# Kernel optimization log

Measured on AMD Instinct MI355X. Metric: run time of the kernel, lower is better.

The kernel has to match this reference:

```python
import jax, jax.numpy as jnp
import numpy as np

B, S, HID, NH, HD, RD, RATIO = 2, 4096, 2048, 16, 128, 64, 4
THETA = 10000.0


def _rope_tables(positions, rd, theta):
    # Unique per-pair frequencies: first half of the Llama cat([freqs, freqs], -1).
    half = rd // 2
    inv_freq = 1.0 / (theta ** (jnp.arange(half, dtype=jnp.float32) / half))
    ang = positions.astype(jnp.float32)[:, None] * inv_freq[None, :]  # [L, half]
    return jnp.cos(ang), jnp.sin(ang)


def _apply_partial_rope_interleaved(x, cos, sin, rd):
    # x: [B, H, L, D]; rotate last rd dims, pairs (2k, 2k+1). cos/sin: [L, rd//2]
    nope, rope = x[..., :-rd], x[..., -rd:]
    pr = rope.reshape(rope.shape[:-1] + (rd // 2, 2))
    a, b = pr[..., 0], pr[..., 1]
    c = cos[None, None]  # [1,1,L,half]
    s = sin[None, None]
    new = jnp.stack([a * c - b * s, a * s + b * c], axis=-1).reshape(rope.shape)
    return jnp.concatenate([nope, new], axis=-1)


def _pool_overlap(kv, gate, ape, ratio, hd):
    # kv/gate: [B, L, 2*hd]; ape: [ratio, 2*hd]. Softmax-gated sum-pool with
    # cross-window overlap: each window pools 2*ratio raw slots (prev window's
    # first-half features + current window's second-half features).
    b, length, feat = kv.shape
    n_w = length // ratio
    kv_w = kv.reshape(b, n_w, ratio, feat)
    gate_w = gate.reshape(b, n_w, ratio, feat) + ape

    def remap(t, fill):
        cur = t[..., hd:]                          # [b, n_w, ratio, hd]
        prev = t[:, :-1, :, :hd]                   # window N-1 first half
        pad = jnp.full((b, 1, ratio, hd), fill, t.dtype)
        prev = jnp.concatenate([pad, prev], axis=1)
        return jnp.concatenate([prev, cur], axis=2)  # [b, n_w, 2*ratio, hd]

    kv_o = remap(kv_w, 0.0)
    gate_o = remap(gate_w, -jnp.inf)
    w = jax.nn.softmax(gate_o, axis=2)
    return (kv_o * w).sum(axis=2)  # [b, n_w, hd]


def setup_inputs() -> dict:
    key = jax.random.key(0)
    ks = jax.random.split(key, 7)
    sc = lambda d: 1.0 / np.sqrt(d)
    return {
        "hidden": jax.random.normal(ks[0], (B, S, HID), jnp.float32),
        "wq": jax.random.normal(ks[1], (HID, NH * HD), jnp.float32) * sc(HID),
        "wkv": jax.random.normal(ks[2], (HID, 2 * HD), jnp.float32) * sc(HID),
        "wgate": jax.random.normal(ks[3], (HID, 2 * HD), jnp.float32) * sc(HID),
        "ape": jax.random.normal(ks[4], (RATIO, 2 * HD), jnp.float32) * 0.02,
        "sinks": jax.random.normal(ks[5], (NH,), jnp.float32) * 0.02,
        "wo": jax.random.normal(ks[6], (NH * HD, HID), jnp.float32) * sc(NH * HD),
        "ratio": RATIO,
        "head_dim": HD,
        "rope_head_dim": RD,
        "num_heads": NH,
    }


def reference(hidden, wq, wkv, wgate, ape, sinks, wo, ratio, head_dim, rope_head_dim, num_heads):
    b, s, _ = hidden.shape
    scale = head_dim ** -0.5

    # Projections
    q = (hidden @ wq).reshape(b, s, num_heads, head_dim).transpose(0, 2, 1, 3)  # [b,h,s,d]
    kv = hidden @ wkv      # [b, s, 2*d]
    gate = hidden @ wgate  # [b, s, 2*d]

    # Overlap gated pooling -> compressed shared KV  [b, n_w, d]
    pooled = _pool_overlap(kv, gate, ape, ratio, head_dim)
    n_w = pooled.shape[1]

    # Partial interleaved RoPE; pooled positions = w * ratio (pool_base = 0)
    q_pos = jnp.arange(s)
    k_pos = jnp.arange(n_w) * ratio
    cq, sq = _rope_tables(q_pos, rope_head_dim, THETA)
    ck, sk = _rope_tables(k_pos, rope_head_dim, THETA)
    q_rot = _apply_partial_rope_interleaved(q, cq, sq, rope_head_dim)
    k_rot = _apply_partial_rope_interleaved(pooled[:, None], ck, sk, rope_head_dim)[:, 0]  # [b,n_w,d]
    v = pooled  # [b, n_w, d]

    # Causal mask over compressed windows: query t sees window w iff its last
    # raw token (w+1)*ratio - 1 <= t.
    mask = jnp.where(q_pos[:, None] >= k_pos[None, :] + ratio - 1, 0.0, -jnp.inf)  # [s, n_w]

    scores = jnp.einsum("bhqd,bkd->bhqk", q_rot, k_rot) * scale + mask[None, None]
    sink_col = jnp.broadcast_to(sinks.reshape(1, num_heads, 1, 1), (b, num_heads, s, 1))
    combined = jnp.concatenate([scores, sink_col], axis=-1)
    probs = jax.nn.softmax(combined - jax.lax.stop_gradient(combined.max(axis=-1, keepdims=True)), axis=-1)[..., :-1]

    attn = jnp.einsum("bhqk,bkd->bhqd", probs, v)               # [b,h,s,d]
    out = attn.transpose(0, 2, 1, 3).reshape(b, s, num_heads * head_dim) @ wo
    return out
```

## Files before the change

kernel.cpp:

```cpp
#include <hip/hip_runtime.h>
#include <math.h>

typedef unsigned short u16;
typedef unsigned int   u32;
typedef __bf16 bf16x8 __attribute__((ext_vector_type(8)));
typedef float  f32x4  __attribute__((ext_vector_type(4)));

#define S_LEN 4096
#define HID   2048
#define NHEAD 16
#define HD    128
#define NW    1024
#define TOK   8192
#define LN10000 9.2103403719761836f
#define NEG_BIG (-1e30f)

__device__ __forceinline__ float b2f(u16 u){
  union { u32 i; float f; } v; v.i = ((u32)u) << 16; return v.f;
}
__device__ __forceinline__ u16 f2b(float f){
  union { float f; u32 i; } v; v.f = f;
  return (u16)((v.i + 0x7FFFu + ((v.i >> 16) & 1u)) >> 16);
}

__global__ __launch_bounds__(256) void cvt_bf16(const float* __restrict__ in,
                                                u16* __restrict__ out){
  size_t i = (size_t)blockIdx.x*256 + threadIdx.x;
  float4 a = ((const float4*)in)[2*i];
  float4 b = ((const float4*)in)[2*i+1];
  u16 t[8];
  t[0]=f2b(a.x); t[1]=f2b(a.y); t[2]=f2b(a.z); t[3]=f2b(a.w);
  t[4]=f2b(b.x); t[5]=f2b(b.y); t[6]=f2b(b.z); t[7]=f2b(b.w);
  *(uint4*)&out[i*8] = *(uint4*)t;
}

__global__ __launch_bounds__(256) void transpose_w(const float* __restrict__ in,
    u16* __restrict__ out, int K, int N){
  __shared__ float t[32][33];
  const int n0 = blockIdx.x*32, k0 = blockIdx.y*32;
  const int c = threadIdx.x & 31, r8 = threadIdx.x >> 5;
  #pragma unroll
  for (int i = 0; i < 4; i++)
    t[r8 + i*8][c] = in[(size_t)(k0 + r8 + i*8)*N + n0 + c];
  __syncthreads();
  #pragma unroll
  for (int i = 0; i < 4; i++)
    out[(size_t)(n0 + r8 + i*8)*K + k0 + c] = f2b(t[c][r8 + i*8]);
}

typedef __attribute__((address_space(3))) u16 as3_u16;
typedef __attribute__((address_space(1))) const u16 as1_u16;
__device__ __forceinline__ void gload16(const u16* g, u16* l){
  __builtin_amdgcn_global_load_lds((as1_u16*)g, (as3_u16*)l, 16, 0, 0);
}

template<typename TC>
__global__ __launch_bounds__(512, 1) void gemm256(const u16* __restrict__ A,
    const u16* __restrict__ Bt, TC* __restrict__ C, int M, int N, int K)
{
  __shared__ __align__(16) u16 LA[2][256*64];
  __shared__ __align__(16) u16 LB[2][256*64];
  const int tid  = threadIdx.x;
  const int lane = tid & 63;
  const int w    = tid >> 6;
  const int wm   = w & 1;
  const int wn   = w >> 1;
  const int lrw  = lane & 15;
  const int quad = lane >> 4;
  const int NB   = N >> 8;
  const int nwg  = gridDim.x;
  const int bid  = blockIdx.x;
  const int swz  = (bid & 7) * (nwg >> 3) + (bid >> 3);
  const int bN   = (swz % NB) << 8;
  const int bM   = (swz / NB) << 8;

  const int rlo = lane >> 3;
  const int csw = ((lane & 7) ^ rlo) << 3;
  const int sr0 = w * 16;
  const int swr = (lrw & 7) << 3;
  const u16* Ag = A  + (size_t)bM * K + (size_t)rlo * K + csw;
  const u16* Bg = Bt + (size_t)bN * K + (size_t)rlo * K + csw;
  const size_t rK = (size_t)K;

  f32x4 acc[8][4];
  #pragma unroll
  for (int i = 0; i < 8; i++)
    #pragma unroll
    for (int j = 0; j < 4; j++)
      #pragma unroll
      for (int r = 0; r < 4; r++) acc[i][j][r] = 0.f;

  const int NT = K >> 6;

  gload16(Ag + (size_t)(  0 + sr0    )*rK, &LA[0][(  0 + sr0    )*64]);
  gload16(Ag + (size_t)(  0 + sr0 + 8)*rK, &LA[0][(  0 + sr0 + 8)*64]);
  gload16(Bg + (size_t)(  0 + sr0    )*rK, &LB[0][(  0 + sr0    )*64]);
  gload16(Bg + (size_t)(  0 + sr0 + 8)*rK, &LB[0][(  0 + sr0 + 8)*64]);
  gload16(Bg + (size_t)(128 + sr0    )*rK, &LB[0][(128 + sr0    )*64]);
  gload16(Bg + (size_t)(128 + sr0 + 8)*rK, &LB[0][(128 + sr0 + 8)*64]);
  gload16(Ag + (size_t)(128 + sr0    )*rK, &LA[0][(128 + sr0    )*64]);
  gload16(Ag + (size_t)(128 + sr0 + 8)*rK, &LA[0][(128 + sr0 + 8)*64]);
  asm volatile("s_waitcnt vmcnt(2)" ::: "memory");
  __builtin_amdgcn_s_barrier();
  __builtin_amdgcn_sched_barrier(0);

  for (int t = 0; t < NT; ++t){
    const int cur = t & 1, nxt = cur ^ 1;
    const int kn  = ((t + 1) & (NT - 1)) << 6;
    const u16* la = &LA[cur][0];
    const u16* lb = &LB[cur][0];
    u16* sa = &LA[nxt][0];
    u16* sb = &LB[nxt][0];

    bf16x8 bfr[4][2], afr[2][2];

    gload16(Ag + (size_t)(  0 + sr0    )*rK + kn, &sa[(  0 + sr0    )*64]);
    gload16(Ag + (size_t)(  0 + sr0 + 8)*rK + kn, &sa[(  0 + sr0 + 8)*64]);
    gload16(Bg + (size_t)(  0 + sr0    )*rK + kn, &sb[(  0 + sr0    )*64]);
    gload16(Bg + (size_t)(  0 + sr0 + 8)*rK + kn, &sb[(  0 + sr0 + 8)*64]);
    #pragma unroll
    for (int nf = 0; nf < 4; nf++)
      #pragma unroll
      for (int kh = 0; kh < 2; kh++)
        bfr[nf][kh] = *(const bf16x8*)&lb[(wn*16 + nf*64 + lrw)*64 + ((kh*32 + quad*8) ^ swr)];
    #pragma unroll
    for (int i = 0; i < 2; i++)
      #pragma unroll
      for (int kh = 0; kh < 2; kh++)
        afr[i][kh] = *(const bf16x8*)&la[(wm*16 + (0+i)*32 + lrw)*64 + ((kh*32 + quad*8) ^ swr)];
    __builtin_amdgcn_s_barrier();
    __builtin_amdgcn_sched_barrier(0);
    __builtin_amdgcn_s_setprio(1);
    #pragma unroll
    for (int i = 0; i < 2; i++)
      #pragma unroll
      for (int nf = 0; nf < 4; nf++)
        #pragma unroll
        for (int kh = 0; kh < 2; kh++)
          acc[0+i][nf] = __builtin_amdgcn_mfma_f32_16x16x32_bf16(afr[i][kh], bfr[nf][kh], acc[0+i][nf], 0, 0, 0);
    __builtin_amdgcn_s_setprio(0);
    __builtin_amdgcn_s_barrier();
    __builtin_amdgcn_sched_barrier(0);

    gload16(Bg + (size_t)(128 + sr0    )*rK + kn, &sb[(128 + sr0    )*64]);
    gload16(Bg + (size_t)(128 + sr0 + 8)*rK + kn, &sb[(128 + sr0 + 8)*64]);
    #pragma unroll
    for (int i = 0; i < 2; i++)
      #pragma unroll
      for (int kh = 0; kh < 2; kh++)
        afr[i][kh] = *(const bf16x8*)&la[(wm*16 + (2+i)*32 + lrw)*64 + ((kh*32 + quad*8) ^ swr)];
    asm volatile("s_waitcnt vmcnt(6)" ::: "memory");
    __builtin_amdgcn_s_barrier();
    __builtin_amdgcn_sched_barrier(0);
    __builtin_amdgcn_s_setprio(1);
    #pragma unroll
    for (int i = 0; i < 2; i++)
      #pragma unroll
      for (int nf = 0; nf < 4; nf++)
        #pragma unroll
        for (int kh = 0; kh < 2; kh++)
          acc[2+i][nf] = __builtin_amdgcn_mfma_f32_16x16x32_bf16(afr[i][kh], bfr[nf][kh], acc[2+i][nf], 0, 0, 0);
    __builtin_amdgcn_s_setprio(0);
    __builtin_amdgcn_s_barrier();
    __builtin_amdgcn_sched_barrier(0);

    gload16(Ag + (size_t)(128 + sr0    )*rK + kn, &sa[(128 + sr0    )*64]);
    gload16(Ag + (size_t)(128 + sr0 + 8)*rK + kn, &sa[(128 + sr0 + 8)*64]);
    #pragma unroll
    for (int i = 0; i < 2; i++)
      #pragma unroll
      for (int kh = 0; kh < 2; kh++)
        afr[i][kh] = *(const bf16x8*)&la[(wm*16 + (4+i)*32 + lrw)*64 + ((kh*32 + quad*8) ^ swr)];
    __builtin_amdgcn_s_barrier();
    __builtin_amdgcn_sched_barrier(0);
    __builtin_amdgcn_s_setprio(1);
    #pragma unroll
    for (int i = 0; i < 2; i++)
      #pragma unroll
      for (int nf = 0; nf < 4; nf++)
        #pragma unroll
        for (int kh = 0; kh < 2; kh++)
          acc[4+i][nf] = __builtin_amdgcn_mfma_f32_16x16x32_bf16(afr[i][kh], bfr[nf][kh], acc[4+i][nf], 0, 0, 0);
    __builtin_amdgcn_s_setprio(0);
    __builtin_amdgcn_s_barrier();
    __builtin_amdgcn_sched_barrier(0);

    #pragma unroll
    for (int i = 0; i < 2; i++)
      #pragma unroll
      for (int kh = 0; kh < 2; kh++)
        afr[i][kh] = *(const bf16x8*)&la[(wm*16 + (6+i)*32 + lrw)*64 + ((kh*32 + quad*8) ^ swr)];
    asm volatile("s_waitcnt vmcnt(2)" ::: "memory");
    __builtin_amdgcn_s_barrier();
    __builtin_amdgcn_sched_barrier(0);
    __builtin_amdgcn_s_setprio(1);
    #pragma unroll
    for (int i = 0; i < 2; i++)
      #pragma unroll
      for (int nf = 0; nf < 4; nf++)
        #pragma unroll
        for (int kh = 0; kh < 2; kh++)
          acc[6+i][nf] = __builtin_amdgcn_mfma_f32_16x16x32_bf16(afr[i][kh], bfr[nf][kh], acc[6+i][nf], 0, 0, 0);
    __builtin_amdgcn_s_setprio(0);
    __builtin_amdgcn_s_barrier();
    __builtin_amdgcn_sched_barrier(0);
  }

  asm volatile("s_waitcnt vmcnt(0)" ::: "memory");

  #pragma unroll
  for (int mf = 0; mf < 8; mf++){
    const int orow0 = bM + wm*16 + mf*32 + quad*4;
    #pragma unroll
    for (int nf = 0; nf < 4; nf++){
      const int ocol = bN + wn*16 + nf*64 + lrw;
      #pragma unroll
      for (int r = 0; r < 4; r++){
        size_t idx = (size_t)(orow0 + r)*N + ocol;
        if constexpr (sizeof(TC) == 4) C[idx] = acc[mf][nf][r];
        else                           C[idx] = f2b(acc[mf][nf][r]);
      }
    }
  }
}

template<typename TC>
__global__ __launch_bounds__(256) void gemm_bf16(const u16* __restrict__ A,
    const u16* __restrict__ Bt, TC* __restrict__ C, int M, int N, int K)
{
  __shared__ u16 As[128*32];
  __shared__ u16 Bs[128*32];
  const int tid  = threadIdx.x;
  const int bM   = blockIdx.y * 128;
  const int bN   = blockIdx.x * 128;
  const int lane = tid & 63;
  const int w    = tid >> 6;
  const int wm   = w >> 1, wn = w & 1;
  const int lrow = lane & 15, quad = lane >> 4;
  const int srow = lane >> 2, skc = (lane & 3) * 8;

  const u16* Ab = &A [(size_t)(bM + w*32 + srow)*K + skc];
  const u16* Bb = &Bt[(size_t)(bN + w*32 + srow)*K + skc];
  const size_t row16 = (size_t)16 * K;

  f32x4 acc[4][4];
  #pragma unroll
  for (int i = 0; i < 4; i++)
    #pragma unroll
    for (int j = 0; j < 4; j++)
      #pragma unroll
      for (int r = 0; r < 4; r++) acc[i][j][r] = 0.f;

  for (int k0 = 0; k0 < K; k0 += 32){
    gload16(Ab + k0,         &As[(w*32     )*32]);
    gload16(Ab + k0 + row16, &As[(w*32 + 16)*32]);
    gload16(Bb + k0,         &Bs[(w*32     )*32]);
    gload16(Bb + k0 + row16, &Bs[(w*32 + 16)*32]);
    __syncthreads();

    bf16x8 af[4], bfv[4];
    #pragma unroll
    for (int mf = 0; mf < 4; mf++)
      af[mf] = *(const bf16x8*)&As[(wm*64 + mf*16 + lrow)*32 + quad*8];
    #pragma unroll
    for (int nf = 0; nf < 4; nf++)
      bfv[nf] = *(const bf16x8*)&Bs[(wn*64 + nf*16 + lrow)*32 + quad*8];
    #pragma unroll
    for (int mf = 0; mf < 4; mf++)
      #pragma unroll
      for (int nf = 0; nf < 4; nf++)
        acc[mf][nf] = __builtin_amdgcn_mfma_f32_16x16x32_bf16(af[mf], bfv[nf], acc[mf][nf], 0, 0, 0);
    __syncthreads();
  }
  #pragma unroll
  for (int mf = 0; mf < 4; mf++){
    #pragma unroll
    for (int nf = 0; nf < 4; nf++){
      int gcol = bN + wn*64 + nf*16 + lrow;
      #pragma unroll
      for (int r = 0; r < 4; r++){
        int grow = bM + wm*64 + mf*16 + quad*4 + r;
        size_t idx = (size_t)grow*N + gcol;
        if constexpr (sizeof(TC) == 4) C[idx] = acc[mf][nf][r];
        else                           C[idx] = f2b(acc[mf][nf][r]);
      }
    }
  }
}

template<typename TA, typename TC>
__global__ __launch_bounds__(256) void gemm_any(const TA* __restrict__ A,
    const float* __restrict__ Bw, TC* __restrict__ C, int M, int N, int K)
{
  __shared__ u16 As[128*40];
  __shared__ u16 Bs[128*40];
  const int tid  = threadIdx.x;
  const int bM   = blockIdx.y * 128;
  const int bN   = blockIdx.x * 128;
  const int lane = tid & 63;
  const int wid  = tid >> 6;
  const int wm   = wid >> 1, wn = wid & 1;
  const int lrow = lane & 15, quad = lane >> 4;

  f32x4 acc[4][4];
  #pragma unroll
  for (int i = 0; i < 4; i++)
    #pragma unroll
    for (int j = 0; j < 4; j++)
      #pragma unroll
      for (int r = 0; r < 4; r++) acc[i][j][r] = 0.f;

  for (int k0 = 0; k0 < K; k0 += 32){
    #pragma unroll
    for (int i = 0; i < 4; i++){
      int c = tid + i*256;
      int row = c >> 3, kc = (c & 7) * 4;
      u16 tmp[4];
      if constexpr (sizeof(TA) == 4){
        float4 v = *(const float4*)&A[(size_t)(bM + row)*K + k0 + kc];
        tmp[0] = f2b(v.x); tmp[1] = f2b(v.y); tmp[2] = f2b(v.z); tmp[3] = f2b(v.w);
      } else {
        *(uint2*)tmp = *(const uint2*)&A[(size_t)(bM + row)*K + k0 + kc];
      }
      *(uint2*)&As[row*40 + kc] = *(uint2*)tmp;
    }
    #pragma unroll
    for (int i = 0; i < 4; i++){
      int c = tid + i*256;
      int kr = c >> 5, nc = (c & 31) * 4;
      float4 v = *(const float4*)&Bw[(size_t)(k0 + kr)*N + bN + nc];
      Bs[(nc+0)*40 + kr] = f2b(v.x);
      Bs[(nc+1)*40 + kr] = f2b(v.y);
      Bs[(nc+2)*40 + kr] = f2b(v.z);
      Bs[(nc+3)*40 + kr] = f2b(v.w);
    }
    __syncthreads();
    bf16x8 af[4], bfv[4];
    #pragma unroll
    for (int mf = 0; mf < 4; mf++)
      af[mf] = *(const bf16x8*)&As[(wm*64 + mf*16 + lrow)*40 + quad*8];
    #pragma unroll
    for (int nf = 0; nf < 4; nf++)
      bfv[nf] = *(const bf16x8*)&Bs[(wn*64 + nf*16 + lrow)*40 + quad*8];
    #pragma unroll
    for (int mf = 0; mf < 4; mf++)
      #pragma unroll
      for (int nf = 0; nf < 4; nf++)
        acc[mf][nf] = __builtin_amdgcn_mfma_f32_16x16x32_bf16(af[mf], bfv[nf], acc[mf][nf], 0, 0, 0);
    __syncthreads();
  }
  #pragma unroll
  for (int mf = 0; mf < 4; mf++){
    #pragma unroll
    for (int nf = 0; nf < 4; nf++){
      int gcol = bN + wn*64 + nf*16 + lrow;
      #pragma unroll
      for (int r = 0; r < 4; r++){
        int grow = bM + wm*64 + mf*16 + quad*4 + r;
        size_t idx = (size_t)grow*N + gcol;
        if constexpr (sizeof(TC) == 4) C[idx] = acc[mf][nf][r];
        else                           C[idx] = f2b(acc[mf][nf][r]);
      }
    }
  }
}

__global__ void pool_rope_k(const u16* __restrict__ kv, const u16* __restrict__ gate,
                            const float* __restrict__ ape, u16* __restrict__ krot,
                            u16* __restrict__ vT, int str){
  const int d = threadIdx.x;
  const int w = blockIdx.x;
  const int b = blockIdx.y;
  __shared__ float sh[HD];
  const bool hasprev = (w > 0);
  float gc[4], vc[4], gp[4], vp[4];
  float m = NEG_BIG;
  #pragma unroll
  for (int r = 0; r < 4; r++){
    size_t t = (size_t)(b*S_LEN + w*4 + r)*str;
    vc[r] = b2f(kv[t + 128 + d]);
    gc[r] = b2f(gate[t + 128 + d]) + ape[r*256 + 128 + d];
    m = fmaxf(m, gc[r]);
  }
  if (hasprev){
    #pragma unroll
    for (int r = 0; r < 4; r++){
      size_t t = (size_t)(b*S_LEN + (w-1)*4 + r)*str;
      vp[r] = b2f(kv[t + d]);
      gp[r] = b2f(gate[t + d]) + ape[r*256 + d];
      m = fmaxf(m, gp[r]);
    }
  }
  float s = 0.f, acc = 0.f;
  #pragma unroll
  for (int r = 0; r < 4; r++){
    float e = __expf(gc[r] - m); s += e; acc += e*vc[r];
  }
  if (hasprev){
    #pragma unroll
    for (int r = 0; r < 4; r++){
      float e = __expf(gp[r] - m); s += e; acc += e*vp[r];
    }
  }
  float pooled = acc / s;
  sh[d] = pooled;
  __syncthreads();
  float kr = pooled;
  if (d >= 64){
    int i = (d - 64) >> 1;
    float freq = expf(-(float)i * (LN10000 / 32.f));
    float ang = (float)(4*w) * freq;
    float sn, cs;
    sincosf(ang, &sn, &cs);
    if ((d & 1) == 0) kr = sh[d]*cs - sh[d+1]*sn;
    else              kr = sh[d-1]*sn + sh[d]*cs;
  }
  krot[(size_t)(b*NW + w)*HD + d] = f2b(kr);
  vT[(size_t)(b*HD + d)*NW + w]   = f2b(pooled);
}

#define AQT 128
#define AKT 64
#define AKSTR 136
#define AVSTR 72
#define APSTR 72
#define ATT_SCALE 0.088388347648318447f

__global__ __launch_bounds__(256, 2) void attn_kernel(
    const u16* __restrict__ qbuf, const u16* __restrict__ krot,
    const u16* __restrict__ vT, const float* __restrict__ sinks,
    u16* __restrict__ attnbuf)
{
  __shared__ u16 Ks[AKT*AKSTR];
  __shared__ u16 Vt[HD*AVSTR];
  __shared__ u16 Pq[AQT*APSTR];

  const int tid  = threadIdx.x;
  const int q0   = (int)(gridDim.x - 1 - blockIdx.x) * AQT;
  const int h    = blockIdx.y;
  const int b    = blockIdx.z;
  const int lane = tid & 63;
  const int wq   = tid >> 6;
  const int lrw  = lane & 15;
  const int quad = lane >> 4;
  const int qg0  = q0 + wq*32 + lrw;

  bf16x8 qf[2][4];
  #pragma unroll
  for (int g = 0; g < 2; g++){
    const u16* qrow = &qbuf[(size_t)(b*S_LEN + qg0 + g*16)*HID + h*HD];
    qf[g][0] = *(const bf16x8*)&qrow[0*32 + quad*8];
    qf[g][1] = *(const bf16x8*)&qrow[1*32 + quad*8];
    const float pos = (float)(qg0 + g*16);
    #pragma unroll
    for (int d0 = 2; d0 < 4; d0++){
      u16 raw[8];
      *(uint4*)raw = *(const uint4*)&qrow[d0*32 + quad*8];
      u16 outv[8];
      #pragma unroll
      for (int pr = 0; pr < 4; pr++){
        int i = (d0 - 2)*16 + quad*4 + pr;
        float fr = expf(-(float)i * (LN10000/32.f));
        float sn, cs;
        sincosf(pos * fr, &sn, &cs);
        float a  = b2f(raw[2*pr]);
        float bb = b2f(raw[2*pr + 1]);
        outv[2*pr]     = f2b(a*cs - bb*sn);
        outv[2*pr + 1] = f2b(a*sn + bb*cs);
      }
      qf[g][d0] = *(bf16x8*)outv;
    }
  }

  float m_run[2] = {NEG_BIG, NEG_BIG};
  float l_run[2] = {0.f, 0.f};
  f32x4 accO[2][8];
  #pragma unroll
  for (int g = 0; g < 2; g++)
    #pragma unroll
    for (int ds = 0; ds < 8; ds++)
      #pragma unroll
      for (int r = 0; r < 4; r++) accO[g][ds][r] = 0.f;

  const int kmax_tile = (q0 + AQT - 1 - 3) >> 2;
  int nchunk = (kmax_tile >> 6) + 1;
  if (nchunk > NW/AKT) nchunk = NW/AKT;

  for (int ch = 0; ch < nchunk; ch++){
    const int kc0 = ch * AKT;
    #pragma unroll
    for (int i = 0; i < 4; i++){
      int c = tid + i*256;
      int kl = c >> 4, cc = (c & 15) * 8;
      *(uint4*)&Ks[kl*AKSTR + cc] =
        *(const uint4*)&krot[(size_t)(b*NW + kc0 + kl)*HD + cc];
    }
    #pragma unroll
    for (int i = 0; i < 4; i++){
      int c = tid + i*256;
      int dv = c >> 3, cc = (c & 7) * 8;
      *(uint4*)&Vt[dv*AVSTR + cc] =
        *(const uint4*)&vT[(size_t)(b*HD + dv)*NW + kc0 + cc];
    }
    __syncthreads();

    f32x4 accS[2][4];
    #pragma unroll
    for (int g = 0; g < 2; g++)
      #pragma unroll
      for (int ks = 0; ks < 4; ks++)
        #pragma unroll
        for (int r = 0; r < 4; r++) accS[g][ks][r] = 0.f;
    #pragma unroll
    for (int d0 = 0; d0 < 4; d0++){
      #pragma unroll
      for (int ks = 0; ks < 4; ks++){
        bf16x8 kf = *(const bf16x8*)&Ks[(ks*16 + lrw)*AKSTR + d0*32 + quad*8];
        accS[0][ks] = __builtin_amdgcn_mfma_f32_16x16x32_bf16(kf, qf[0][d0], accS[0][ks], 0, 0, 0);
        accS[1][ks] = __builtin_amdgcn_mfma_f32_16x16x32_bf16(kf, qf[1][d0], accS[1][ks], 0, 0, 0);
      }
    }

    float alpha[2];
    #pragma unroll
    for (int g = 0; g < 2; g++){
      const int qg = qg0 + g*16;
      float p[16];
      float lmax = NEG_BIG;
      #pragma unroll
      for (int ks = 0; ks < 4; ks++)
        #pragma unroll
        for (int r = 0; r < 4; r++){
          int kg = kc0 + ks*16 + quad*4 + r;
          float s = (qg >= 4*kg + 3) ? accS[g][ks][r]*ATT_SCALE : NEG_BIG;
          p[ks*4 + r] = s;
          lmax = fmaxf(lmax, s);
        }
      lmax = fmaxf(lmax, __shfl_xor(lmax, 16));
      lmax = fmaxf(lmax, __shfl_xor(lmax, 32));
      float mnew = fmaxf(m_run[g], lmax);
      alpha[g] = __expf(m_run[g] - mnew);
      m_run[g] = mnew;
      float ls = 0.f;
      #pragma unroll
      for (int i = 0; i < 16; i++){
        float e = __expf(p[i] - mnew);
        p[i] = e; ls += e;
      }
      ls += __shfl_xor(ls, 16);
      ls += __shfl_xor(ls, 32);
      l_run[g] = l_run[g]*alpha[g] + ls;
      #pragma unroll
      for (int ks = 0; ks < 4; ks++){
        u16 pb[4];
        #pragma unroll
        for (int r = 0; r < 4; r++) pb[r] = f2b(p[ks*4 + r]);
        *(uint2*)&Pq[(wq*32 + g*16 + lrw)*APSTR + ks*16 + quad*4] = *(uint2*)pb;
      }
    }

    #pragma unroll
    for (int g = 0; g < 2; g++)
      #pragma unroll
      for (int ds = 0; ds < 8; ds++)
        #pragma unroll
        for (int r = 0; r < 4; r++) accO[g][ds][r] *= alpha[g];

    #pragma unroll
    for (int kks = 0; kks < 2; kks++){
      bf16x8 pf0 = *(const bf16x8*)&Pq[(wq*32      + lrw)*APSTR + kks*32 + quad*8];
      bf16x8 pf1 = *(const bf16x8*)&Pq[(wq*32 + 16 + lrw)*APSTR + kks*32 + quad*8];
      #pragma unroll
      for (int ds = 0; ds < 8; ds++){
        bf16x8 av = *(const bf16x8*)&Vt[(ds*16 + lrw)*AVSTR + kks*32 + quad*8];
        accO[0][ds] = __builtin_amdgcn_mfma_f32_16x16x32_bf16(av, pf0, accO[0][ds], 0, 0, 0);
        accO[1][ds] = __builtin_amdgcn_mfma_f32_16x16x32_bf16(av, pf1, accO[1][ds], 0, 0, 0);
      }
    }
    __syncthreads();
  }

  const float snk = sinks[h];
  #pragma unroll
  for (int g = 0; g < 2; g++){
    float mf = fmaxf(m_run[g], snk);
    float em = __expf(m_run[g] - mf);
    float sc = em / (l_run[g]*em + __expf(snk - mf));
    size_t o = (size_t)(b*S_LEN + qg0 + g*16)*HID + h*HD;
    #pragma unroll
    for (int ds = 0; ds < 8; ds++){
      u16 ob[4];
      #pragma unroll
      for (int r = 0; r < 4; r++) ob[r] = f2b(accO[g][ds][r] * sc);
      *(uint2*)&attnbuf[o + ds*16 + quad*4] = *(uint2*)ob;
    }
  }
}

extern "C" void kernel_launch(void* const* d_in, const int* in_sizes, int n_in,
                              void* d_out, int out_size, void* d_ws, size_t ws_size,
                              hipStream_t stream)
{
  const float* hidden = (const float*)d_in[0];
  const float* wq     = (const float*)d_in[1];
  const float* wkv    = (const float*)d_in[2];
  const float* wgate  = (const float*)d_in[3];
  const float* ape    = (const float*)d_in[4];
  const float* sinks  = (const float*)d_in[5];
  const float* wo     = (const float*)d_in[6];

  const size_t NEED = ((size_t)TOK*HID*2 + (size_t)TOK*512 + (size_t)4*NW*HD
                     + (size_t)HID*HID + (size_t)512*HID) * sizeof(u16);

  if (ws_size >= NEED){
    u16* hid_bf = (u16*)d_ws;
    u16* qbuf   = hid_bf + (size_t)TOK*HID;
    u16* kvg    = qbuf   + (size_t)TOK*HID;
    u16* krot   = kvg    + (size_t)TOK*512;
    u16* vTb    = krot   + (size_t)2*NW*HD;
    u16* wqT    = vTb    + (size_t)2*NW*HD;
    u16* wkvgT  = wqT    + (size_t)HID*HID;
    u16* attnbuf = hid_bf;
    u16* woT     = kvg;

    cvt_bf16<<<(TOK*HID/8)/256, 256, 0, stream>>>(hidden, hid_bf);
    transpose_w<<<dim3(HID/32, HID/32), 256, 0, stream>>>(wq, wqT, HID, HID);
    transpose_w<<<dim3(256/32, HID/32), 256, 0, stream>>>(wkv,   wkvgT,            HID, 256);
    transpose_w<<<dim3(256/32, HID/32), 256, 0, stream>>>(wgate, wkvgT + (size_t)256*HID, HID, 256);
    gemm256<u16><<<dim3((TOK/256)*(HID/256)), 512, 0, stream>>>(hid_bf, wqT, qbuf, TOK, HID, HID);
    gemm_bf16<u16><<<dim3(512/128, TOK/128), 256, 0, stream>>>(hid_bf, wkvgT, kvg,  TOK, 512, HID);
    pool_rope_k<<<dim3(NW, 2), 128, 0, stream>>>(kvg, kvg + 256, ape, krot, vTb, 512);
    attn_kernel<<<dim3(S_LEN/AQT, NHEAD, 2), 256, 0, stream>>>(qbuf, krot, vTb, sinks, attnbuf);
    transpose_w<<<dim3(HID/32, HID/32), 256, 0, stream>>>(wo, woT, HID, HID);
    gemm256<float><<<dim3((TOK/256)*(HID/256)), 512, 0, stream>>>(attnbuf, woT, (float*)d_out, TOK, HID, HID);
  } else {
    u16* qbuf    = (u16*)d_ws;
    u16* kvbuf   = qbuf    + (size_t)TOK*HID;
    u16* gatebuf = kvbuf   + (size_t)TOK*256;
    u16* krot    = gatebuf + (size_t)TOK*256;
    u16* vTb     = krot    + (size_t)2*NW*HD;
    u16* attnbuf = vTb     + (size_t)2*NW*HD;

    gemm_any<float,u16><<<dim3(HID/128, TOK/128), 256, 0, stream>>>(hidden, wq,    qbuf,    TOK, HID, HID);
    gemm_any<float,u16><<<dim3(256/128, TOK/128), 256, 0, stream>>>(hidden, wkv,   kvbuf,   TOK, 256, HID);
    gemm_any<float,u16><<<dim3(256/128, TOK/128), 256, 0, stream>>>(hidden, wgate, gatebuf, TOK, 256, HID);
    pool_rope_k<<<dim3(NW, 2), 128, 0, stream>>>(kvbuf, gatebuf, ape, krot, vTb, 256);
    attn_kernel<<<dim3(S_LEN/AQT, NHEAD, 2), 256, 0, stream>>>(qbuf, krot, vTb, sinks, attnbuf);
    gemm_any<u16,float><<<dim3(HID/128, TOK/128), 256, 0, stream>>>(attnbuf, wo, (float*)d_out, TOK, HID, HID);
  }
}
```

Measured before the change: 500.3 us.

## Use direct global-to-LDS loads with XOR swizzle and skip masking in attention

The K and V^T tiles in the attention kernel are now copied straight from global memory into LDS with gload16. The padded LDS strides are replaced by an XOR swizzle on 16-byte chunks, and the MFMA fragment reads are updated to match. The MFMA sections are wrapped in s_setprio raise and lower calls. The causal mask comparison is skipped for chunks that lie entirely below the diagonal. Together these aim to cut register staging, LDS bank conflicts and per-element mask work, but they depend on the swizzle index math matching the direct-load lane layout exactly.

Measured after the change: 494.6 us. About the same (-1.1%).

```diff
diff --git a/kernel.cpp b/kernel.cpp
--- a/kernel.cpp
+++ b/kernel.cpp
@@ -421,8 +421,6 @@
 
 #define AQT 128
 #define AKT 64
-#define AKSTR 136
-#define AVSTR 72
 #define APSTR 72
 #define ATT_SCALE 0.088388347648318447f
 
@@ -431,8 +429,8 @@
     const u16* __restrict__ vT, const float* __restrict__ sinks,
     u16* __restrict__ attnbuf)
 {
-  __shared__ u16 Ks[AKT*AKSTR];
-  __shared__ u16 Vt[HD*AVSTR];
+  __shared__ __align__(16) u16 Ks[AKT*128];
+  __shared__ __align__(16) u16 Vt[HD*64];
   __shared__ u16 Pq[AQT*APSTR];
 
   const int tid  = threadIdx.x;
@@ -444,6 +442,12 @@
   const int lrw  = lane & 15;
   const int quad = lane >> 4;
   const int qg0  = q0 + wq*32 + lrw;
+  const int swl  = lrw & 7;
+
+  const int krow_l = lane >> 4;
+  const int kc16   = lane & 15;
+  const int vrow_l = lane >> 3;
+  const int vc16   = lane & 7;
 
   bf16x8 qf[2][4];
   #pragma unroll
@@ -490,17 +494,15 @@
     const int kc0 = ch * AKT;
     #pragma unroll
     for (int i = 0; i < 4; i++){
-      int c = tid + i*256;
-      int kl = c >> 4, cc = (c & 15) * 8;
-      *(uint4*)&Ks[kl*AKSTR + cc] =
-        *(const uint4*)&krot[(size_t)(b*NW + kc0 + kl)*HD + cc];
+      int row = wq*16 + i*4 + krow_l;
+      int c16s = kc16 ^ (row & 7);
+      gload16(&krot[(size_t)(b*NW + kc0 + row)*HD + c16s*8], &Ks[(wq*16 + i*4)*128]);
     }
     #pragma unroll
     for (int i = 0; i < 4; i++){
-      int c = tid + i*256;
-      int dv = c >> 3, cc = (c & 7) * 8;
-      *(uint4*)&Vt[dv*AVSTR + cc] =
-        *(const uint4*)&vT[(size_t)(b*HD + dv)*NW + kc0 + cc];
+      int row = wq*32 + i*8 + vrow_l;
+      int c16s = vc16 ^ (row & 7);
+      gload16(&vT[(size_t)(b*HD + row)*NW + kc0 + c16s*8], &Vt[(wq*32 + i*8)*64]);
     }
     __syncthreads();
 
@@ -511,31 +513,45 @@
       for (int ks = 0; ks < 4; ks++)
         #pragma unroll
         for (int r = 0; r < 4; r++) accS[g][ks][r] = 0.f;
+    __builtin_amdgcn_s_setprio(1);
     #pragma unroll
     for (int d0 = 0; d0 < 4; d0++){
       #pragma unroll
       for (int ks = 0; ks < 4; ks++){
-        bf16x8 kf = *(const bf16x8*)&Ks[(ks*16 + lrw)*AKSTR + d0*32 + quad*8];
+        bf16x8 kf = *(const bf16x8*)&Ks[(ks*16 + lrw)*128 + (((4*d0 + quad) ^ swl) << 3)];
         accS[0][ks] = __builtin_amdgcn_mfma_f32_16x16x32_bf16(kf, qf[0][d0], accS[0][ks], 0, 0, 0);
         accS[1][ks] = __builtin_amdgcn_mfma_f32_16x16x32_bf16(kf, qf[1][d0], accS[1][ks], 0, 0, 0);
       }
     }
-
+    __builtin_amdgcn_s_setprio(0);
+
+    const bool needmask = (q0 < 4*(kc0 + AKT - 1) + 3);
     float alpha[2];
     #pragma unroll
     for (int g = 0; g < 2; g++){
       const int qg = qg0 + g*16;
       float p[16];
       float lmax = NEG_BIG;
-      #pragma unroll
-      for (int ks = 0; ks < 4; ks++)
-        #pragma unroll
-        for (int r = 0; r < 4; r++){
-          int kg = kc0 + ks*16 + quad*4 + r;
-          float s = (qg >= 4*kg + 3) ? accS[g][ks][r]*ATT_SCALE : NEG_BIG;
-          p[ks*4 + r] = s;
-          lmax = fmaxf(lmax, s);
-        }
+      if (needmask){
+        #pragma unroll
+        for (int ks = 0; ks < 4; ks++)
+          #pragma unroll
+          for (int r = 0; r < 4; r++){
+            int kg = kc0 + ks*16 + quad*4 + r;
+            float s = (qg >= 4*kg + 3) ? accS[g][ks][r]*ATT_SCALE : NEG_BIG;
+            p[ks*4 + r] = s;
+            lmax = fmaxf(lmax, s);
+          }
+      } else {
+        #pragma unroll
+        for (int ks = 0; ks < 4; ks++)
+          #pragma unroll
+          for (int r = 0; r < 4; r++){
+            float s = accS[g][ks][r]*ATT_SCALE;
+            p[ks*4 + r] = s;
+            lmax = fmaxf(lmax, s);
+          }
+      }
       lmax = fmaxf(lmax, __shfl_xor(lmax, 16));
       lmax = fmaxf(lmax, __shfl_xor(lmax, 32));
       float mnew = fmaxf(m_run[g], lmax);
@@ -566,17 +582,19 @@
         #pragma unroll
         for (int r = 0; r < 4; r++) accO[g][ds][r] *= alpha[g];
 
+    __builtin_amdgcn_s_setprio(1);
     #pragma unroll
     for (int kks = 0; kks < 2; kks++){
       bf16x8 pf0 = *(const bf16x8*)&Pq[(wq*32      + lrw)*APSTR + kks*32 + quad*8];
       bf16x8 pf1 = *(const bf16x8*)&Pq[(wq*32 + 16 + lrw)*APSTR + kks*32 + quad*8];
       #pragma unroll
       for (int ds = 0; ds < 8; ds++){
-        bf16x8 av = *(const bf16x8*)&Vt[(ds*16 + lrw)*AVSTR + kks*32 + quad*8];
+        bf16x8 av = *(const bf16x8*)&Vt[(ds*16 + lrw)*64 + (((kks*4 + quad) ^ swl) << 3)];
         accO[0][ds] = __builtin_amdgcn_mfma_f32_16x16x32_bf16(av, pf0, accO[0][ds], 0, 0, 0);
         accO[1][ds] = __builtin_amdgcn_mfma_f32_16x16x32_bf16(av, pf1, accO[1][ds], 0, 0, 0);
       }
     }
+    __builtin_amdgcn_s_setprio(0);
     __syncthreads();
   }
 
```
